# Kernel tuning notes

Measured on AMD Instinct MI355X. Metric: run time of the kernel, lower is better.

The kernel has to match this reference:

```python
import jax, jax.numpy as jnp
import numpy as np

B, T, IN, OUT, H = 1024, 25, 96, 96, 2048


def setup_inputs() -> dict:
    key = jax.random.key(0)
    ks = jax.random.split(key, 16)
    s = 0.05  # small init scale to keep gates in linear-ish region
    return {
        "input": jax.random.normal(ks[0], (B, IN), jnp.float32),
        "future_poses": jax.random.normal(ks[1], (B, T, OUT), jnp.float32),
        "hiddens": jax.random.normal(ks[2], (2, B, H), jnp.float32) * s,
        "W_ih0": jax.random.normal(ks[3], (3 * H, IN), jnp.float32) * s,
        "W_hh0": jax.random.normal(ks[4], (3 * H, H), jnp.float32) * s,
        "b_ih0": jax.random.normal(ks[5], (3 * H,), jnp.float32) * s,
        "b_hh0": jax.random.normal(ks[6], (3 * H,), jnp.float32) * s,
        "W_ih1": jax.random.normal(ks[7], (3 * H, H), jnp.float32) * s,
        "W_hh1": jax.random.normal(ks[8], (3 * H, H), jnp.float32) * s,
        "b_ih1": jax.random.normal(ks[9], (3 * H,), jnp.float32) * s,
        "b_hh1": jax.random.normal(ks[10], (3 * H,), jnp.float32) * s,
        "W_fc": jax.random.normal(ks[11], (OUT, H), jnp.float32) * s,
        "b_fc": jax.random.normal(ks[12], (OUT,), jnp.float32) * s,
        "teacher_forcing_rate": 0,
    }


def gru_cell(x, h, W_ih, W_hh, b_ih, b_hh):
    # PyTorch nn.GRUCell math; gate order [r, z, n]
    gi = x @ W_ih.T + b_ih
    gh = h @ W_hh.T + b_hh
    i_r, i_z, i_n = jnp.split(gi, 3, axis=-1)
    h_r, h_z, h_n = jnp.split(gh, 3, axis=-1)
    r = jax.nn.sigmoid(i_r + h_r)
    z = jax.nn.sigmoid(i_z + h_z)
    n = jnp.tanh(i_n + r * h_n)
    return (1.0 - z) * n + z * h


def reference(input, future_poses, hiddens, W_ih0, W_hh0, b_ih0, b_hh0,
              W_ih1, W_hh1, b_ih1, b_hh1, W_fc, b_fc, teacher_forcing_rate):
    # dropout p=0.0 (eval) -> identity; teacher_forcing_rate=0 -> always
    def step(carry, _):
        dec_in, h0, h1 = carry
        h0 = gru_cell(dec_in, h0, W_ih0, W_hh0, b_ih0, b_hh0)
        h1 = gru_cell(h0, h1, W_ih1, W_hh1, b_ih1, b_hh1)
        out = jax.nn.sigmoid(h1 @ W_fc.T + b_fc)  # [B, OUT]
        dec_in = jax.lax.stop_gradient(out)       # torch .detach()
        return (dec_in, h0, h1), out

    carry0 = (input, hiddens[0], hiddens[1])
    _, outs = jax.lax.scan(step, carry0, None, length=T)  # [T, B, OUT]
    return jnp.transpose(outs, (1, 0, 2))  # [B, T, OUT]
```

## Files before the change

kernel.cpp:

```cpp
#include <hip/hip_runtime.h>
#include <stdint.h>

typedef __bf16 bf16;
typedef __attribute__((ext_vector_type(8))) __bf16 bf16x8;
typedef __attribute__((ext_vector_type(4))) float f32x4;

#define GRU_H 2048
#define ODIM 96
#define PADX 128
#define BATCH 1024
#define TSTEPS 25

__device__ __forceinline__ float sigm(float x) { return 1.f / (1.f + __expf(-x)); }

__device__ __forceinline__ void gload16(const void* g, void* l) {
  __builtin_amdgcn_global_load_lds((const __attribute__((address_space(1))) uint32_t*)g,
                                   (__attribute__((address_space(3))) uint32_t*)l, 16, 0, 0);
}

__global__ void k_cvt(const float* __restrict__ s, bf16* __restrict__ d, int n) {
  int stride = gridDim.x * blockDim.x;
  for (int i = blockIdx.x * blockDim.x + threadIdx.x; i < n; i += stride)
    d[i] = (bf16)s[i];
}

__global__ void k_cvt_pad(const float* __restrict__ s, bf16* __restrict__ d,
                          int rows, int cin, int cout) {
  int n = rows * cout;
  int stride = gridDim.x * blockDim.x;
  for (int i = blockIdx.x * blockDim.x + threadIdx.x; i < n; i += stride) {
    int r = i / cout, c = i - r * cout;
    d[i] = (c < cin) ? (bf16)s[r * cin + c] : (bf16)0.f;
  }
}

__global__ void k_init_h(const float* __restrict__ s, float* __restrict__ hf,
                         bf16* __restrict__ hb, int n) {
  int stride = gridDim.x * blockDim.x;
  for (int i = blockIdx.x * blockDim.x + threadIdx.x; i < n; i += stride) {
    float v = s[i];
    hf[i] = v;
    hb[i] = (bf16)v;
  }
}

__global__ __launch_bounds__(512, 1) void k_gru(
    const bf16* __restrict__ xb, int kx,
    const bf16* __restrict__ hb,
    const bf16* __restrict__ wih,
    const bf16* __restrict__ whh,
    const float* __restrict__ bih, const float* __restrict__ bhh,
    const float* __restrict__ hprevf,
    float* __restrict__ hnewf, bf16* __restrict__ hnewb) {
  __shared__ alignas(16) char sm[3][40960];

  const int tid = threadIdx.x;
  const int l = tid & 63;
  const int w = tid >> 6;
  const int wm = w & 1, wn = w >> 1;
  const int wb = tid & ~63;
  const int bn0 = blockIdx.x * 64;
  const int bm0 = blockIdx.y * 128;
  const int lm = l >> 4, ln = l & 15;
  char* sm0 = &sm[0][0];

  const int S1 = GRU_H / 64;
  const int S2 = kx / 64;
  const int S = S1 + S2;

  f32x4 accR[4] = {};
  f32x4 accZ[4] = {};
  f32x4 accNH[4] = {};
  f32x4 accNI[4] = {};

  const bf16* pAhh[2]; const bf16* pAih[2]; int ldsA[2];
  const bf16* pWhh[3]; const bf16* pWih[3]; int ldsB[3];
#pragma unroll
  for (int i = 0; i < 2; ++i) {
    int c = i * 512 + tid, row = c >> 3, slot = (c & 7) ^ (row & 7);
    pAhh[i] = hb + (size_t)(bm0 + row) * GRU_H + slot * 8;
    pAih[i] = xb + (size_t)(bm0 + row) * kx + slot * 8;
    ldsA[i] = (i * 512 + wb) << 4;
  }
#pragma unroll
  for (int i = 0; i < 3; ++i) {
    int c = i * 512 + tid, row = c >> 3, slot = (c & 7) ^ (row & 7);
    int g = row >> 6, r = row & 63;
    pWhh[i] = whh + (size_t)(g * GRU_H + bn0 + r) * GRU_H + slot * 8;
    pWih[i] = wih + (size_t)(g * GRU_H + bn0 + r) * kx + slot * 8;
    ldsB[i] = 16384 + ((i * 512 + wb) << 4);
  }

  auto stageP = [&](const bf16* const (&pa)[2], const bf16* const (&pw)[3],
                    int koff, char* sb) {
#pragma unroll
    for (int i = 0; i < 2; ++i) gload16(pa[i] + koff, sb + ldsA[i]);
#pragma unroll
    for (int i = 0; i < 3; ++i) gload16(pw[i] + koff, sb + ldsB[i]);
  };
  auto stageSel = [&](int sp, char* sb) {
    if (sp < S1) stageP(pAhh, pWhh, sp * 64, sb);
    else         stageP(pAih, pWih, (sp - S1) * 64, sb);
  };

  auto computeStep = [&](const char* bp, f32x4 (&accN)[4]) {
#pragma unroll
    for (int kf = 0; kf < 2; ++kf) {
      bf16x8 af[4];
#pragma unroll
      for (int mf = 0; mf < 4; ++mf) {
        int row = wm * 64 + mf * 16 + ln;
        int pos = (kf * 4 + lm) ^ (row & 7);
        af[mf] = *(const bf16x8*)(bp + row * 128 + (pos << 4));
      }
#pragma unroll
      for (int g = 0; g < 3; ++g) {
        int row = g * 64 + wn * 16 + ln;
        int pos = (kf * 4 + lm) ^ (row & 7);
        bf16x8 bq = *(const bf16x8*)(bp + 16384 + row * 128 + (pos << 4));
        f32x4* accG = (g == 0) ? accR : (g == 1) ? accZ : accN;
#pragma unroll
        for (int mf = 0; mf < 4; ++mf)
          accG[mf] = __builtin_amdgcn_mfma_f32_16x16x32_bf16(af[mf], bq, accG[mf], 0, 0, 0);
      }
    }
  };

  auto body = [&](int s, char* bufR, char* bufW) {
    asm volatile("s_waitcnt vmcnt(5) lgkmcnt(0)\ns_barrier" ::: "memory");
    if (s + 2 < S) stageSel(s + 2, bufW);
    __builtin_amdgcn_s_setprio(1);
    if (s < S1) computeStep(bufR, accNH);
    else        computeStep(bufR, accNI);
    __builtin_amdgcn_s_setprio(0);
  };

  stageSel(0, sm0);
  stageSel(1, sm0 + 40960);

  const int SM1 = S - 1;
  for (int s = 0; s < SM1; s += 3) {
    body(s + 0, sm0,         sm0 + 81920);
    body(s + 1, sm0 + 40960, sm0);
    body(s + 2, sm0 + 81920, sm0 + 40960);
  }
  asm volatile("s_waitcnt vmcnt(0) lgkmcnt(0)\ns_barrier" ::: "memory");
  __builtin_amdgcn_s_setprio(1);
  computeStep(sm0, accNI);
  __builtin_amdgcn_s_setprio(0);

  {
    int j = bn0 + wn * 16 + ln;
    float br = bih[j] + bhh[j];
    float bz = bih[GRU_H + j] + bhh[GRU_H + j];
    float bin = bih[2 * GRU_H + j];
    float bhn = bhh[2 * GRU_H + j];
#pragma unroll
    for (int mf = 0; mf < 4; ++mf) {
#pragma unroll
      for (int rr = 0; rr < 4; ++rr) {
        int m = bm0 + wm * 64 + mf * 16 + lm * 4 + rr;
        size_t idx = (size_t)m * GRU_H + j;
        float hp = hprevf[idx];
        float rg = sigm(accR[mf][rr] + br);
        float zg = sigm(accZ[mf][rr] + bz);
        float ng = tanhf(accNI[mf][rr] + bin + rg * (accNH[mf][rr] + bhn));
        float hn = (1.f - zg) * ng + zg * hp;
        hnewf[idx] = hn;
        hnewb[idx] = (bf16)hn;
      }
    }
  }
}

__global__ __launch_bounds__(256, 1) void k_fc_part(const bf16* __restrict__ h1b,
                                                    const bf16* __restrict__ wfc,
                                                    float* __restrict__ part) {
  const int kc = blockIdx.x;
  const int mt = blockIdx.y;
  const int l = threadIdx.x & 63, w = threadIdx.x >> 6;
  const int lm = l >> 4, ln = l & 15;
  const int m0 = mt * 64 + w * 16;
  const int k0 = kc * 128;
  f32x4 acc[6] = {};
#pragma unroll
  for (int kf = 0; kf < 4; ++kf) {
    bf16x8 a = *(const bf16x8*)&h1b[(size_t)(m0 + ln) * GRU_H + k0 + kf * 32 + lm * 8];
#pragma unroll
    for (int nf = 0; nf < 6; ++nf) {
      bf16x8 b = *(const bf16x8*)&wfc[(size_t)(nf * 16 + ln) * GRU_H + k0 + kf * 32 + lm * 8];
      acc[nf] = __builtin_amdgcn_mfma_f32_16x16x32_bf16(a, b, acc[nf], 0, 0, 0);
    }
  }
  float* base = part + (size_t)kc * (BATCH * ODIM);
#pragma unroll
  for (int nf = 0; nf < 6; ++nf)
#pragma unroll
    for (int rr = 0; rr < 4; ++rr)
      base[(size_t)(m0 + lm * 4 + rr) * ODIM + nf * 16 + ln] = acc[nf][rr];
}

__global__ void k_fc_red(const float* __restrict__ part, const float* __restrict__ bfc,
                         float* __restrict__ dout, bf16* __restrict__ decb, int t) {
  int i = blockIdx.x * blockDim.x + threadIdx.x;
  if (i >= BATCH * ODIM) return;
  int m = i / ODIM, n = i - m * ODIM;
  float s = bfc[n];
#pragma unroll
  for (int kc = 0; kc < 16; ++kc) s += part[(size_t)kc * (BATCH * ODIM) + i];
  s = sigm(s);
  dout[(size_t)m * (TSTEPS * ODIM) + t * ODIM + n] = s;
  decb[m * PADX + n] = (bf16)s;
}

extern "C" void kernel_launch(void* const* d_in, const int* in_sizes, int n_in,
                              void* d_out, int out_size, void* d_ws, size_t ws_size,
                              hipStream_t stream) {
  const float* input   = (const float*)d_in[0];
  const float* hiddens = (const float*)d_in[2];
  const float* W_ih0   = (const float*)d_in[3];
  const float* W_hh0   = (const float*)d_in[4];
  const float* b_ih0   = (const float*)d_in[5];
  const float* b_hh0   = (const float*)d_in[6];
  const float* W_ih1   = (const float*)d_in[7];
  const float* W_hh1   = (const float*)d_in[8];
  const float* b_ih1   = (const float*)d_in[9];
  const float* b_hh1   = (const float*)d_in[10];
  const float* W_fc    = (const float*)d_in[11];
  const float* b_fc    = (const float*)d_in[12];
  float* out = (float*)d_out;

  char* p = (char*)d_ws;
  auto take = [&](size_t n) { char* q = p; p += (n + 255) & ~(size_t)255; return q; };
  bf16* wih0b = (bf16*)take((size_t)3 * GRU_H * PADX * 2);
  bf16* whh0b = (bf16*)take((size_t)3 * GRU_H * GRU_H * 2);
  bf16* wih1b = (bf16*)take((size_t)3 * GRU_H * GRU_H * 2);
  bf16* whh1b = (bf16*)take((size_t)3 * GRU_H * GRU_H * 2);
  bf16* wfcb  = (bf16*)take((size_t)ODIM * GRU_H * 2);
  bf16* decb  = (bf16*)take((size_t)BATCH * PADX * 2);
  float* h0f[2], *h1f[2];
  bf16* h0b[2], *h1b[2];
  h0f[0] = (float*)take((size_t)BATCH * GRU_H * 4);
  h0f[1] = (float*)take((size_t)BATCH * GRU_H * 4);
  h1f[0] = (float*)take((size_t)BATCH * GRU_H * 4);
  h1f[1] = (float*)take((size_t)BATCH * GRU_H * 4);
  h0b[0] = (bf16*)take((size_t)BATCH * GRU_H * 2);
  h0b[1] = (bf16*)take((size_t)BATCH * GRU_H * 2);
  h1b[0] = (bf16*)take((size_t)BATCH * GRU_H * 2);
  h1b[1] = (bf16*)take((size_t)BATCH * GRU_H * 2);
  float* fcpart = (float*)take((size_t)16 * BATCH * ODIM * 4);

  k_cvt_pad<<<768, 256, 0, stream>>>(W_ih0, wih0b, 3 * GRU_H, ODIM, PADX);
  k_cvt<<<2048, 256, 0, stream>>>(W_hh0, whh0b, 3 * GRU_H * GRU_H);
  k_cvt<<<2048, 256, 0, stream>>>(W_ih1, wih1b, 3 * GRU_H * GRU_H);
  k_cvt<<<2048, 256, 0, stream>>>(W_hh1, whh1b, 3 * GRU_H * GRU_H);
  k_cvt<<<192, 256, 0, stream>>>(W_fc, wfcb, ODIM * GRU_H);
  k_cvt_pad<<<512, 256, 0, stream>>>(input, decb, BATCH, ODIM, PADX);
  k_init_h<<<2048, 256, 0, stream>>>(hiddens, h0f[0], h0b[0], BATCH * GRU_H);
  k_init_h<<<2048, 256, 0, stream>>>(hiddens + (size_t)BATCH * GRU_H, h1f[0], h1b[0], BATCH * GRU_H);

  int cur = 0;
  for (int t = 0; t < TSTEPS; ++t) {
    int nxt = cur ^ 1;
    k_gru<<<dim3(32, 8), 512, 0, stream>>>(decb, PADX, h0b[cur], wih0b, whh0b,
                                           b_ih0, b_hh0, h0f[cur], h0f[nxt], h0b[nxt]);
    k_gru<<<dim3(32, 8), 512, 0, stream>>>(h0b[nxt], GRU_H, h1b[cur], wih1b, whh1b,
                                           b_ih1, b_hh1, h1f[cur], h1f[nxt], h1b[nxt]);
    k_fc_part<<<dim3(16, 16), 256, 0, stream>>>(h1b[nxt], wfcb, fcpart);
    k_fc_red<<<384, 256, 0, stream>>>(fcpart, b_fc, out, decb, t);
    cur = nxt;
  }
}
```

Before: 2.566 ms.

## Halve GRU block to 4 waves with 64x32 per-wave tiles

The GRU GEMM block shrinks from 512 to 256 threads while keeping the 128x64 block tile and the 3-stage LDS ring. Each wave now covers 32 output columns per gate instead of 16, so each A fragment loaded from LDS feeds two MFMAs and LDS read traffic per MFMA drops. The global-to-LDS staging is rewritten to issue 10 loads per thread, with the wait count adjusted to match. The cost is twice as many accumulator registers per thread and only one wave per SIMD, which leaves less room to hide latency.

```diff
diff --git a/kernel.cpp b/kernel.cpp
--- a/kernel.cpp
+++ b/kernel.cpp
@@ -44,7 +44,7 @@
   }
 }
 
-__global__ __launch_bounds__(512, 1) void k_gru(
+__global__ __launch_bounds__(256, 1) void k_gru(
     const bf16* __restrict__ xb, int kx,
     const bf16* __restrict__ hb,
     const bf16* __restrict__ wih,
@@ -68,75 +68,86 @@
   const int S2 = kx / 64;
   const int S = S1 + S2;
 
-  f32x4 accR[4] = {};
-  f32x4 accZ[4] = {};
-  f32x4 accNH[4] = {};
-  f32x4 accNI[4] = {};
-
-  const bf16* pAhh[2]; const bf16* pAih[2]; int ldsA[2];
-  const bf16* pWhh[3]; const bf16* pWih[3]; int ldsB[3];
-#pragma unroll
-  for (int i = 0; i < 2; ++i) {
-    int c = i * 512 + tid, row = c >> 3, slot = (c & 7) ^ (row & 7);
-    pAhh[i] = hb + (size_t)(bm0 + row) * GRU_H + slot * 8;
-    pAih[i] = xb + (size_t)(bm0 + row) * kx + slot * 8;
-    ldsA[i] = (i * 512 + wb) << 4;
-  }
-#pragma unroll
-  for (int i = 0; i < 3; ++i) {
-    int c = i * 512 + tid, row = c >> 3, slot = (c & 7) ^ (row & 7);
-    int g = row >> 6, r = row & 63;
-    pWhh[i] = whh + (size_t)(g * GRU_H + bn0 + r) * GRU_H + slot * 8;
-    pWih[i] = wih + (size_t)(g * GRU_H + bn0 + r) * kx + slot * 8;
-    ldsB[i] = 16384 + ((i * 512 + wb) << 4);
-  }
-
-  auto stageP = [&](const bf16* const (&pa)[2], const bf16* const (&pw)[3],
-                    int koff, char* sb) {
-#pragma unroll
-    for (int i = 0; i < 2; ++i) gload16(pa[i] + koff, sb + ldsA[i]);
-#pragma unroll
-    for (int i = 0; i < 3; ++i) gload16(pw[i] + koff, sb + ldsB[i]);
-  };
-  auto stageSel = [&](int sp, char* sb) {
-    if (sp < S1) stageP(pAhh, pWhh, sp * 64, sb);
-    else         stageP(pAih, pWih, (sp - S1) * 64, sb);
-  };
-
-  auto computeStep = [&](const char* bp, f32x4 (&accN)[4]) {
+  f32x4 accR[4][2] = {};
+  f32x4 accZ[4][2] = {};
+  f32x4 accNH[4][2] = {};
+  f32x4 accNI[4][2] = {};
+
+  const int row0 = tid >> 3;
+  const int slot = (tid & 7) ^ (row0 & 7);
+  const char* hbB  = (const char*)hb;
+  const char* xbB  = (const char*)xb;
+  const char* whhB = (const char*)whh;
+  const char* wihB = (const char*)wih;
+  const size_t colb = (size_t)slot * 16;
+  const size_t aHH = (size_t)(bm0 + row0) * (GRU_H * 2) + colb;
+  const size_t aIH = (size_t)(bm0 + row0) * ((size_t)kx * 2) + colb;
+  const size_t bHH = (size_t)(bn0 + row0) * (GRU_H * 2) + colb;
+  const size_t bIH = (size_t)(bn0 + row0) * ((size_t)kx * 2) + colb;
+
+  auto stageHH = [&](int k0, char* sb) {
+    size_t kb = (size_t)k0 * 2;
+#pragma unroll
+    for (int i = 0; i < 4; ++i)
+      gload16(hbB + aHH + (size_t)i * (32 * GRU_H * 2) + kb,
+              sb + ((i * 256 + wb) << 4));
+#pragma unroll
+    for (int i = 0; i < 6; ++i)
+      gload16(whhB + bHH + (size_t)(i >> 1) * ((size_t)GRU_H * GRU_H * 2)
+                         + (size_t)(i & 1) * (32 * GRU_H * 2) + kb,
+              sb + 16384 + ((i * 256 + wb) << 4));
+  };
+  auto stageIH = [&](int k0, char* sb) {
+    size_t kb = (size_t)k0 * 2;
+#pragma unroll
+    for (int i = 0; i < 4; ++i)
+      gload16(xbB + aIH + (size_t)i * ((size_t)32 * kx * 2) + kb,
+              sb + ((i * 256 + wb) << 4));
+#pragma unroll
+    for (int i = 0; i < 6; ++i)
+      gload16(wihB + bIH + (size_t)(i >> 1) * ((size_t)GRU_H * kx * 2)
+                         + (size_t)(i & 1) * ((size_t)32 * kx * 2) + kb,
+              sb + 16384 + ((i * 256 + wb) << 4));
+  };
+
+  auto computeStep = [&](const char* bp, f32x4 (&accN)[4][2]) {
 #pragma unroll
     for (int kf = 0; kf < 2; ++kf) {
+      const int pos = ((kf * 4 + lm) ^ (ln & 7)) << 4;
       bf16x8 af[4];
 #pragma unroll
-      for (int mf = 0; mf < 4; ++mf) {
-        int row = wm * 64 + mf * 16 + ln;
-        int pos = (kf * 4 + lm) ^ (row & 7);
-        af[mf] = *(const bf16x8*)(bp + row * 128 + (pos << 4));
+      for (int mf = 0; mf < 4; ++mf)
+        af[mf] = *(const bf16x8*)(bp + (wm * 64 + mf * 16 + ln) * 128 + pos);
+#pragma unroll
+      for (int g = 0; g < 3; ++g) {
+        bf16x8 bq[2];
+#pragma unroll
+        for (int jf = 0; jf < 2; ++jf)
+          bq[jf] = *(const bf16x8*)(bp + 16384 + (g * 64 + wn * 32 + jf * 16 + ln) * 128 + pos);
+        f32x4 (*acc)[2] = (g == 0) ? accR : (g == 1) ? accZ : accN;
+#pragma unroll
+        for (int mf = 0; mf < 4; ++mf)
+#pragma unroll
+          for (int jf = 0; jf < 2; ++jf)
+            acc[mf][jf] = __builtin_amdgcn_mfma_f32_16x16x32_bf16(af[mf], bq[jf], acc[mf][jf], 0, 0, 0);
       }
-#pragma unroll
-      for (int g = 0; g < 3; ++g) {
-        int row = g * 64 + wn * 16 + ln;
-        int pos = (kf * 4 + lm) ^ (row & 7);
-        bf16x8 bq = *(const bf16x8*)(bp + 16384 + row * 128 + (pos << 4));
-        f32x4* accG = (g == 0) ? accR : (g == 1) ? accZ : accN;
-#pragma unroll
-        for (int mf = 0; mf < 4; ++mf)
-          accG[mf] = __builtin_amdgcn_mfma_f32_16x16x32_bf16(af[mf], bq, accG[mf], 0, 0, 0);
-      }
     }
   };
 
   auto body = [&](int s, char* bufR, char* bufW) {
-    asm volatile("s_waitcnt vmcnt(5) lgkmcnt(0)\ns_barrier" ::: "memory");
-    if (s + 2 < S) stageSel(s + 2, bufW);
+    asm volatile("s_waitcnt vmcnt(10) lgkmcnt(0)\ns_barrier" ::: "memory");
+    if (s + 2 < S) {
+      if (s + 2 < S1) stageHH((s + 2) * 64, bufW);
+      else            stageIH((s + 2 - S1) * 64, bufW);
+    }
     __builtin_amdgcn_s_setprio(1);
     if (s < S1) computeStep(bufR, accNH);
     else        computeStep(bufR, accNI);
     __builtin_amdgcn_s_setprio(0);
   };
 
-  stageSel(0, sm0);
-  stageSel(1, sm0 + 40960);
+  stageHH(0, sm0);
+  stageHH(64, sm0 + 40960);
 
   const int SM1 = S - 1;
   for (int s = 0; s < SM1; s += 3) {
@@ -149,8 +160,9 @@
   computeStep(sm0, accNI);
   __builtin_amdgcn_s_setprio(0);
 
-  {
-    int j = bn0 + wn * 16 + ln;
+#pragma unroll
+  for (int jf = 0; jf < 2; ++jf) {
+    int j = bn0 + wn * 32 + jf * 16 + ln;
     float br = bih[j] + bhh[j];
     float bz = bih[GRU_H + j] + bhh[GRU_H + j];
     float bin = bih[2 * GRU_H + j];
@@ -162,9 +174,9 @@
         int m = bm0 + wm * 64 + mf * 16 + lm * 4 + rr;
         size_t idx = (size_t)m * GRU_H + j;
         float hp = hprevf[idx];
-        float rg = sigm(accR[mf][rr] + br);
-        float zg = sigm(accZ[mf][rr] + bz);
-        float ng = tanhf(accNI[mf][rr] + bin + rg * (accNH[mf][rr] + bhn));
+        float rg = sigm(accR[mf][jf][rr] + br);
+        float zg = sigm(accZ[mf][jf][rr] + bz);
+        float ng = tanhf(accNI[mf][jf][rr] + bin + rg * (accNH[mf][jf][rr] + bhn));
         float hn = (1.f - zg) * ng + zg * hp;
         hnewf[idx] = hn;
         hnewb[idx] = (bf16)hn;
@@ -262,9 +274,9 @@
   int cur = 0;
   for (int t = 0; t < TSTEPS; ++t) {
     int nxt = cur ^ 1;
-    k_gru<<<dim3(32, 8), 512, 0, stream>>>(decb, PADX, h0b[cur], wih0b, whh0b,
+    k_gru<<<dim3(32, 8), 256, 0, stream>>>(decb, PADX, h0b[cur], wih0b, whh0b,
                                            b_ih0, b_hh0, h0f[cur], h0f[nxt], h0b[nxt]);
-    k_gru<<<dim3(32, 8), 512, 0, stream>>>(h0b[nxt], GRU_H, h1b[cur], wih1b, whh1b,
+    k_gru<<<dim3(32, 8), 256, 0, stream>>>(h0b[nxt], GRU_H, h1b[cur], wih1b, whh1b,
                                            b_ih1, b_hh1, h1f[cur], h1f[nxt], h1b[nxt]);
     k_fc_part<<<dim3(16, 16), 256, 0, stream>>>(h1b[nxt], wfcb, fcpart);
     k_fc_red<<<384, 256, 0, stream>>>(fcpart, b_fc, out, decb, t);
```

New measurement: 3.169 ms. +23.5%, slower.

## Split GRU GEMM main loop into two interleaved half-steps with staged global loads

Applied to the files above, without the earlier changes.

Restructures the GEMM k-loop body into two phases per 64-wide K step. Each phase reads LDS fragments, issues half of the next-stage global-to-LDS loads (A first, then B), and runs 12 MFMAs behind explicit barriers and sched_barriers. This interleaves memory issue with matrix compute in a ping-pong fashion, and it simplifies the LDS swizzle index to use ln instead of row. The cost is extra s_barrier calls per step, plus fragile hand-placed waitcnt values that must match the number of outstanding loads.

```diff
diff --git a/kernel.cpp b/kernel.cpp
--- a/kernel.cpp
+++ b/kernel.cpp
@@ -91,52 +91,83 @@
     ldsB[i] = 16384 + ((i * 512 + wb) << 4);
   }
 
-  auto stageP = [&](const bf16* const (&pa)[2], const bf16* const (&pw)[3],
-                    int koff, char* sb) {
-#pragma unroll
-    for (int i = 0; i < 2; ++i) gload16(pa[i] + koff, sb + ldsA[i]);
-#pragma unroll
-    for (int i = 0; i < 3; ++i) gload16(pw[i] + koff, sb + ldsB[i]);
-  };
-  auto stageSel = [&](int sp, char* sb) {
-    if (sp < S1) stageP(pAhh, pWhh, sp * 64, sb);
-    else         stageP(pAih, pWih, (sp - S1) * 64, sb);
-  };
-
-  auto computeStep = [&](const char* bp, f32x4 (&accN)[4]) {
-#pragma unroll
-    for (int kf = 0; kf < 2; ++kf) {
-      bf16x8 af[4];
-#pragma unroll
-      for (int mf = 0; mf < 4; ++mf) {
-        int row = wm * 64 + mf * 16 + ln;
-        int pos = (kf * 4 + lm) ^ (row & 7);
-        af[mf] = *(const bf16x8*)(bp + row * 128 + (pos << 4));
-      }
-#pragma unroll
-      for (int g = 0; g < 3; ++g) {
-        int row = g * 64 + wn * 16 + ln;
-        int pos = (kf * 4 + lm) ^ (row & 7);
-        bf16x8 bq = *(const bf16x8*)(bp + 16384 + row * 128 + (pos << 4));
-        f32x4* accG = (g == 0) ? accR : (g == 1) ? accZ : accN;
-#pragma unroll
-        for (int mf = 0; mf < 4; ++mf)
-          accG[mf] = __builtin_amdgcn_mfma_f32_16x16x32_bf16(af[mf], bq, accG[mf], 0, 0, 0);
-      }
-    }
+  auto stageA = [&](int sp, char* sb) {
+    if (sp < S1) {
+      int koff = sp * 64;
+#pragma unroll
+      for (int i = 0; i < 2; ++i) gload16(pAhh[i] + koff, sb + ldsA[i]);
+    } else {
+      int koff = (sp - S1) * 64;
+#pragma unroll
+      for (int i = 0; i < 2; ++i) gload16(pAih[i] + koff, sb + ldsA[i]);
+    }
+  };
+  auto stageB = [&](int sp, char* sb) {
+    if (sp < S1) {
+      int koff = sp * 64;
+#pragma unroll
+      for (int i = 0; i < 3; ++i) gload16(pWhh[i] + koff, sb + ldsB[i]);
+    } else {
+      int koff = (sp - S1) * 64;
+#pragma unroll
+      for (int i = 0; i < 3; ++i) gload16(pWih[i] + koff, sb + ldsB[i]);
+    }
+  };
+
+  auto readF = [&](const char* bp, int kf, bf16x8 (&af)[4], bf16x8 (&bq)[3]) {
+    const int pos = ((kf * 4 + lm) ^ (ln & 7)) << 4;
+#pragma unroll
+    for (int mf = 0; mf < 4; ++mf)
+      af[mf] = *(const bf16x8*)(bp + (wm * 64 + mf * 16 + ln) * 128 + pos);
+#pragma unroll
+    for (int g = 0; g < 3; ++g)
+      bq[g] = *(const bf16x8*)(bp + 16384 + (g * 64 + wn * 16 + ln) * 128 + pos);
+  };
+  auto mfma12 = [&](bf16x8 (&af)[4], bf16x8 (&bq)[3], f32x4 (&accN)[4]) {
+#pragma unroll
+    for (int mf = 0; mf < 4; ++mf)
+      accR[mf] = __builtin_amdgcn_mfma_f32_16x16x32_bf16(af[mf], bq[0], accR[mf], 0, 0, 0);
+#pragma unroll
+    for (int mf = 0; mf < 4; ++mf)
+      accZ[mf] = __builtin_amdgcn_mfma_f32_16x16x32_bf16(af[mf], bq[1], accZ[mf], 0, 0, 0);
+#pragma unroll
+    for (int mf = 0; mf < 4; ++mf)
+      accN[mf] = __builtin_amdgcn_mfma_f32_16x16x32_bf16(af[mf], bq[2], accN[mf], 0, 0, 0);
   };
 
   auto body = [&](int s, char* bufR, char* bufW) {
-    asm volatile("s_waitcnt vmcnt(5) lgkmcnt(0)\ns_barrier" ::: "memory");
-    if (s + 2 < S) stageSel(s + 2, bufW);
+    bf16x8 af[4], bq[3];
+    const bool st = (s + 2 < S);
+    const bool isHH = (s < S1);
+    readF(bufR, 0, af, bq);
+    if (st) stageA(s + 2, bufW);
+    asm volatile("s_barrier" ::: "memory");
+    asm volatile("s_waitcnt lgkmcnt(0)" ::: "memory");
+    __builtin_amdgcn_sched_barrier(0);
     __builtin_amdgcn_s_setprio(1);
-    if (s < S1) computeStep(bufR, accNH);
-    else        computeStep(bufR, accNI);
+    if (isHH) mfma12(af, bq, accNH); else mfma12(af, bq, accNI);
     __builtin_amdgcn_s_setprio(0);
-  };
-
-  stageSel(0, sm0);
-  stageSel(1, sm0 + 40960);
+    asm volatile("s_barrier" ::: "memory");
+    readF(bufR, 1, af, bq);
+    if (st) {
+      stageB(s + 2, bufW);
+      asm volatile("s_waitcnt vmcnt(5)" ::: "memory");
+    } else {
+      asm volatile("s_waitcnt vmcnt(0)" ::: "memory");
+    }
+    asm volatile("s_barrier" ::: "memory");
+    asm volatile("s_waitcnt lgkmcnt(0)" ::: "memory");
+    __builtin_amdgcn_sched_barrier(0);
+    __builtin_amdgcn_s_setprio(1);
+    if (isHH) mfma12(af, bq, accNH); else mfma12(af, bq, accNI);
+    __builtin_amdgcn_s_setprio(0);
+    asm volatile("s_barrier" ::: "memory");
+  };
+
+  stageA(0, sm0);        stageB(0, sm0);
+  stageA(1, sm0 + 40960); stageB(1, sm0 + 40960);
+  asm volatile("s_waitcnt vmcnt(5)" ::: "memory");
+  asm volatile("s_barrier" ::: "memory");
 
   const int SM1 = S - 1;
   for (int s = 0; s < SM1; s += 3) {
@@ -144,10 +175,13 @@
     body(s + 1, sm0 + 40960, sm0);
     body(s + 2, sm0 + 81920, sm0 + 40960);
   }
-  asm volatile("s_waitcnt vmcnt(0) lgkmcnt(0)\ns_barrier" ::: "memory");
-  __builtin_amdgcn_s_setprio(1);
-  computeStep(sm0, accNI);
-  __builtin_amdgcn_s_setprio(0);
+  {
+    bf16x8 af[4], bq[3];
+    readF(sm0, 0, af, bq);
+    mfma12(af, bq, accNI);
+    readF(sm0, 1, af, bq);
+    mfma12(af, bq, accNI);
+  }
 
   {
     int j = bn0 + wn * 16 + ln;
```

Measured after the change: 3.748 ms. 1.46x slower.
